# Kernel optimization log

Measured on AMD Instinct MI355X. Metric: run time of the kernel, lower is better.

## Reference

```python
import jax, jax.numpy as jnp
import numpy as np

LPOS, LDIR, H = 10, 4, 256
N = 262144


def posenc(x, L):
    freqs = (2.0 ** jnp.arange(L)).astype(x.dtype)  # [L]
    ang = x[:, None, :] * freqs[:, None]            # [N, L, 3]
    sc = jnp.concatenate([jnp.sin(ang), jnp.cos(ang)], axis=-1)  # [N, L, 6]
    return jnp.concatenate([x, sc.reshape(x.shape[0], L * 6)], axis=1)


def _lin(key, fan_in, fan_out):
    k1, k2 = jax.random.split(key)
    bound = 1.0 / np.sqrt(fan_in)
    w = jax.random.uniform(k1, (fan_out, fan_in), jnp.float32, -bound, bound)
    b = jax.random.uniform(k2, (fan_out,), jnp.float32, -bound, bound)
    return w, b


def setup_inputs() -> dict:
    key = jax.random.key(0)
    ks = jax.random.split(key, 16)
    inp = {
        'xyz': jax.random.normal(ks[0], (N, 3), jnp.float32),
        'd': jax.random.normal(ks[1], (N, 3), jnp.float32),
    }
    in1 = LPOS * 6 + 3  # 63
    dims1 = [(in1, H), (H, H), (H, H), (H, H), (H, H)]
    for i, (fi, fo) in enumerate(dims1):
        w, b = _lin(ks[2 + i], fi, fo)
        inp[f'w1_{i}'], inp[f'b1_{i}'] = w, b
    dims2 = [(H + in1, H), (H, H), (H, H), (H, H + 1)]
    for i, (fi, fo) in enumerate(dims2):
        w, b = _lin(ks[7 + i], fi, fo)
        inp[f'w2_{i}'], inp[f'b2_{i}'] = w, b
    w, b = _lin(ks[11], H + LDIR * 6 + 3, H // 2)
    inp['wr0'], inp['br0'] = w, b
    w, b = _lin(ks[12], H // 2, 3)
    inp['wr1'], inp['br1'] = w, b
    return inp


def reference(xyz, d,
              w1_0, b1_0, w1_1, b1_1, w1_2, b1_2, w1_3, b1_3, w1_4, b1_4,
              w2_0, b2_0, w2_1, b2_1, w2_2, b2_2, w2_3, b2_3,
              wr0, br0, wr1, br1):
    relu = jax.nn.relu
    x_emb = posenc(xyz, LPOS)  # [N, 63]
    d_emb = posenc(d, LDIR)    # [N, 27]
    h = x_emb
    for w, b in ((w1_0, b1_0), (w1_1, b1_1), (w1_2, b1_2), (w1_3, b1_3), (w1_4, b1_4)):
        h = relu(h @ w.T + b)
    h = jnp.concatenate([h, x_emb], axis=1)
    for w, b in ((w2_0, b2_0), (w2_1, b2_1), (w2_2, b2_2)):
        h = relu(h @ w.T + b)
    h = h @ w2_3.T + b2_3  # [N, H+1]
    sigma = h[:, -1]
    h = h[:, :-1]
    # rgb head
    g = relu(jnp.concatenate([h, d_emb], axis=1) @ wr0.T + br0)
    c = jax.nn.sigmoid(g @ wr1.T + br1)  # [N, 3]
    return c, relu(sigma)
```

## Files before the change

kernel.cpp:

```cpp
#include <hip/hip_runtime.h>
#include <hip/hip_bf16.h>

#define NPTS 262144
#define ROWS 64
#define BUF1_OFF 16384
#define XBUF_OFF 32768
#define LDS_BYTES ((16384*2 + 4096)*2)

typedef __attribute__((ext_vector_type(8)))  short short8;
typedef __attribute__((ext_vector_type(4)))  float f32x4;
typedef __attribute__((ext_vector_type(16))) float f32x16;

__device__ __forceinline__ ushort bfu(float f) {
  union { float f; unsigned u; } x; x.f = f;
  unsigned r = x.u + 0x7fffu + ((x.u >> 16) & 1u);
  return (ushort)(r >> 16);
}
__device__ __forceinline__ unsigned pk2(float a, float b) {
  __hip_bfloat162 h = __float22bfloat162_rn(float2{a, b});
  return *reinterpret_cast<unsigned*>(&h);
}

__global__ void pack_w(const float* __restrict__ w, ushort* __restrict__ dst,
                       int OUT, int KIN, int nct, int nkt) {
  int t = blockIdx.x * 256 + threadIdx.x;
  int total = nct * nkt * 64;
  if (t >= total) return;
  int l  = t & 63;
  int kt = (t >> 6) % nkt;
  int ct = (t >> 6) / nkt;
  int row = ct * 32 + (l & 31);
  int k0  = kt * 16 + (l >> 5) * 8;
  ushort* d = dst + (size_t)t * 8;
  #pragma unroll
  for (int j = 0; j < 8; ++j) {
    int k = k0 + j;
    float v = (row < OUT && k < KIN) ? w[(size_t)row * KIN + k] : 0.f;
    d[j] = bfu(v);
  }
}

__global__ void pack_b(const float* __restrict__ b, float* __restrict__ dst, int OUT, int OUTP) {
  int i = blockIdx.x * 256 + threadIdx.x;
  if (i < OUTP) dst[i] = (i < OUT) ? b[i] : 0.f;
}

template<int NKT, int KSPLIT, int NR, bool RELU>
__device__ __forceinline__ void layerg(
    const ushort* __restrict__ wpk, const float* __restrict__ bias,
    const ushort* a0, int s0, const ushort* a1, int s1,
    ushort* dst, int ct, int r2base, int lane)
{
  const int l5 = lane >> 5;
  f32x4 bq[4];
  #pragma unroll
  for (int qq = 0; qq < 4; ++qq)
    bq[qq] = *(const f32x4*)(bias + ct * 32 + qq * 8 + 4 * l5);
  f32x16 acc[NR];
  #pragma unroll
  for (int rr = 0; rr < NR; ++rr)
    #pragma unroll
    for (int qq = 0; qq < 4; ++qq) {
      acc[rr][qq * 4 + 0] = bq[qq][0];
      acc[rr][qq * 4 + 1] = bq[qq][1];
      acc[rr][qq * 4 + 2] = bq[qq][2];
      acc[rr][qq * 4 + 3] = bq[qq][3];
    }
  #pragma unroll
  for (int kt = 0; kt < NKT; ++kt) {
    short8 bv = *(const short8*)(wpk + (size_t)((ct * NKT + kt) * 64 + lane) * 8);
    #pragma unroll
    for (int rr = 0; rr < NR; ++rr) {
      const int r2 = r2base + rr;
      const ushort* src = (kt < KSPLIT)
          ? a0 + (r2 * s0 + kt) * 512 + lane * 8
          : a1 + (r2 * s1 + (kt - KSPLIT)) * 512 + lane * 8;
      short8 av = *(const short8*)src;
      acc[rr] = __builtin_amdgcn_mfma_f32_32x32x16_bf16(bv, av, acc[rr], 0, 0, 0);
    }
  }
  #pragma unroll
  for (int rr = 0; rr < NR; ++rr) {
    const int r2 = r2base + rr;
    #pragma unroll
    for (int qq = 0; qq < 4; ++qq) {
      float v0 = acc[rr][qq * 4 + 0], v1 = acc[rr][qq * 4 + 1];
      float v2 = acc[rr][qq * 4 + 2], v3 = acc[rr][qq * 4 + 3];
      if (RELU) {
        v0 = fmaxf(v0, 0.f); v1 = fmaxf(v1, 0.f);
        v2 = fmaxf(v2, 0.f); v3 = fmaxf(v3, 0.f);
      }
      uint2 p; p.x = pk2(v0, v1); p.y = pk2(v2, v3);
      *(uint2*)(dst + (r2 * 16 + ct * 2 + (qq >> 1)) * 512
                    + ((lane & 31) + 32 * (qq & 1)) * 8 + 4 * l5) = p;
    }
  }
}

__device__ __forceinline__ float pe_val(const float xv[3], int c, int CMAX) {
  if (c < 3) return xv[c];
  if (c < CMAX) {
    int idx = c - 3, l = idx / 6, t = idx - l * 6;
    float f = (float)(1 << l);
    float xx = xv[t < 3 ? t : t - 3];
    return (t < 3) ? __sinf(xx * f) : __cosf(xx * f);
  }
  return 0.f;
}

extern __shared__ ushort smem[];

__global__ __launch_bounds__(512, 4) void nerf_fused(
    const float* __restrict__ xyz, const float* __restrict__ dvec,
    const ushort* __restrict__ wp, const float* __restrict__ bp,
    float* __restrict__ out)
{
  ushort* buf0 = smem;
  ushort* buf1 = smem + BUF1_OFF;
  ushort* xbuf = smem + XBUF_OFF;
  const int tid  = threadIdx.x;
  const int row0 = blockIdx.x * ROWS;
  const int wave = tid >> 6, lane = tid & 63;
  const int l5 = lane >> 5;

  {
    const int r2 = wave >> 2, kt = wave & 3;
    const float* x = xyz + (size_t)(row0 + r2 * 32 + (lane & 31)) * 3;
    float xv[3] = {x[0], x[1], x[2]};
    const int c0 = kt * 16 + l5 * 8;
    unsigned u[4];
    #pragma unroll
    for (int q = 0; q < 4; ++q)
      u[q] = (unsigned)bfu(pe_val(xv, c0 + q * 2, 63))
           | ((unsigned)bfu(pe_val(xv, c0 + q * 2 + 1, 63)) << 16);
    *(uint4*)(xbuf + (r2 * 4 + kt) * 512 + lane * 8) = make_uint4(u[0], u[1], u[2], u[3]);
  }
  __syncthreads();
  layerg<4, 0, 2, true >(wp + 0,      bp + 0,    xbuf, 4, xbuf, 4, buf0, wave, 0, lane);
  __syncthreads();
  layerg<16, 16, 2, true>(wp + 16384,  bp + 256,  buf0, 16, buf0, 16, buf1, wave, 0, lane);
  __syncthreads();
  layerg<16, 16, 2, true>(wp + 81920,  bp + 512,  buf1, 16, buf1, 16, buf0, wave, 0, lane);
  __syncthreads();
  layerg<16, 16, 2, true>(wp + 147456, bp + 768,  buf0, 16, buf0, 16, buf1, wave, 0, lane);
  __syncthreads();
  layerg<16, 16, 2, true>(wp + 212992, bp + 1024, buf1, 16, buf1, 16, buf0, wave, 0, lane);
  __syncthreads();
  layerg<20, 16, 2, true>(wp + 278528, bp + 1280, buf0, 16, xbuf, 4, buf1, wave, 0, lane);
  __syncthreads();
  if (wave < 4) {
    const int r2 = wave >> 1, kt = wave & 1;
    const float* d = dvec + (size_t)(row0 + r2 * 32 + (lane & 31)) * 3;
    float dv[3] = {d[0], d[1], d[2]};
    const int c0 = kt * 16 + l5 * 8;
    unsigned u[4];
    #pragma unroll
    for (int q = 0; q < 4; ++q)
      u[q] = (unsigned)bfu(pe_val(dv, c0 + q * 2, 27))
           | ((unsigned)bfu(pe_val(dv, c0 + q * 2 + 1, 27)) << 16);
    *(uint4*)(xbuf + (r2 * 2 + kt) * 512 + lane * 8) = make_uint4(u[0], u[1], u[2], u[3]);
  }
  layerg<16, 16, 2, true>(wp + 360448, bp + 1536, buf1, 16, buf1, 16, buf0, wave, 0, lane);
  __syncthreads();
  layerg<16, 16, 2, true>(wp + 425984, bp + 1792, buf0, 16, buf0, 16, buf1, wave, 0, lane);
  __syncthreads();
  layerg<16, 16, 2, false>(wp + 491520, bp + 2048, buf1, 16, buf1, 16, buf0, wave, 0, lane);
  if (wave < 2) {
    const ushort* w23 = wp + 491520;
    const int r2 = wave;
    f32x16 acc;
    #pragma unroll
    for (int qq = 0; qq < 4; ++qq) {
      f32x4 b4 = *(const f32x4*)(bp + 2048 + 256 + qq * 8 + 4 * l5);
      acc[qq * 4 + 0] = b4[0]; acc[qq * 4 + 1] = b4[1];
      acc[qq * 4 + 2] = b4[2]; acc[qq * 4 + 3] = b4[3];
    }
    #pragma unroll
    for (int kt = 0; kt < 16; ++kt) {
      short8 bv = *(const short8*)(w23 + (size_t)((8 * 16 + kt) * 64 + lane) * 8);
      short8 av = *(const short8*)(buf1 + (r2 * 16 + kt) * 512 + lane * 8);
      acc = __builtin_amdgcn_mfma_f32_32x32x16_bf16(bv, av, acc, 0, 0, 0);
    }
    if (lane < 32)
      out[(size_t)3 * NPTS + row0 + r2 * 32 + lane] = fmaxf(acc[0], 0.f);
  }
  __syncthreads();
  layerg<18, 16, 1, true>(wp + 565248, bp + 2336, buf0, 16, xbuf, 2, buf1, wave & 3, wave >> 2, lane);
  __syncthreads();
  if (wave < 2) {
    const ushort* w = wp + 602112;
    const int r2 = wave;
    f32x16 acc;
    #pragma unroll
    for (int qq = 0; qq < 4; ++qq) {
      f32x4 b4 = *(const f32x4*)(bp + 2464 + qq * 8 + 4 * l5);
      acc[qq * 4 + 0] = b4[0]; acc[qq * 4 + 1] = b4[1];
      acc[qq * 4 + 2] = b4[2]; acc[qq * 4 + 3] = b4[3];
    }
    #pragma unroll
    for (int kt = 0; kt < 8; ++kt) {
      short8 bv = *(const short8*)(w + (size_t)(kt * 64 + lane) * 8);
      short8 av = *(const short8*)(buf1 + (r2 * 16 + kt) * 512 + lane * 8);
      acc = __builtin_amdgcn_mfma_f32_32x32x16_bf16(bv, av, acc, 0, 0, 0);
    }
    if (lane < 32) {
      int p = row0 + r2 * 32 + lane;
      out[(size_t)p * 3 + 0] = 1.f / (1.f + __expf(-acc[0]));
      out[(size_t)p * 3 + 1] = 1.f / (1.f + __expf(-acc[1]));
      out[(size_t)p * 3 + 2] = 1.f / (1.f + __expf(-acc[2]));
    }
  }
}

extern "C" void kernel_launch(void* const* d_in, const int* in_sizes, int n_in,
                              void* d_out, int out_size, void* d_ws, size_t ws_size,
                              hipStream_t stream) {
  const float* xyz  = (const float*)d_in[0];
  const float* dvec = (const float*)d_in[1];
  ushort* wp = (ushort*)d_ws;
  float*  bp = (float*)((char*)d_ws + 1212416);

  struct WSpec { int idx, OUT, KIN, nct, nkt, off; };
  const WSpec wspecs[11] = {
    { 2, 256,  63, 8,  4,      0},
    { 4, 256, 256, 8, 16,  16384},
    { 6, 256, 256, 8, 16,  81920},
    { 8, 256, 256, 8, 16, 147456},
    {10, 256, 256, 8, 16, 212992},
    {12, 256, 319, 8, 20, 278528},
    {14, 256, 256, 8, 16, 360448},
    {16, 256, 256, 8, 16, 425984},
    {18, 257, 256, 9, 16, 491520},
    {20, 128, 283, 4, 18, 565248},
    {22,   3, 128, 1,  8, 602112},
  };
  for (int i = 0; i < 11; ++i) {
    int total = wspecs[i].nct * wspecs[i].nkt * 64;
    pack_w<<<dim3((total + 255) / 256), dim3(256), 0, stream>>>(
      (const float*)d_in[wspecs[i].idx], wp + wspecs[i].off,
      wspecs[i].OUT, wspecs[i].KIN, wspecs[i].nct, wspecs[i].nkt);
  }
  struct BSpec { int idx, OUT, OUTP, off; };
  const BSpec bspecs[11] = {
    { 3, 256, 256,    0}, { 5, 256, 256,  256}, { 7, 256, 256,  512}, { 9, 256, 256,  768},
    {11, 256, 256, 1024}, {13, 256, 256, 1280}, {15, 256, 256, 1536}, {17, 256, 256, 1792},
    {19, 257, 288, 2048}, {21, 128, 128, 2336}, {23,   3,  32, 2464},
  };
  for (int i = 0; i < 11; ++i) {
    pack_b<<<dim3((bspecs[i].OUTP + 255) / 256), dim3(256), 0, stream>>>(
      (const float*)d_in[bspecs[i].idx], bp + bspecs[i].off, bspecs[i].OUT, bspecs[i].OUTP);
  }

  hipFuncSetAttribute(reinterpret_cast<const void*>(nerf_fused),
                      hipFuncAttributeMaxDynamicSharedMemorySize, LDS_BYTES);
  nerf_fused<<<dim3(NPTS / ROWS), dim3(512), LDS_BYTES, stream>>>(xyz, dvec, wp, bp, (float*)d_out);
}
```

Before: 380.3 us.

## Use 4 waves per block with two column tiles per wave for register reuse

Block size drops from 512 to 256 threads, and each wave now computes two 32-column output tiles for both 32-row groups. Each activation fragment loaded from LDS is reused across two weight tiles, which halves LDS activation reads per MFMA. The cost is twice the accumulator registers per wave (four 16-float accumulators) and fewer waves per block to hide latency. Launch bounds change to (256,2), which may lower occupancy.

```diff
diff --git a/kernel.cpp b/kernel.cpp
--- a/kernel.cpp
+++ b/kernel.cpp
@@ -45,54 +45,64 @@
   if (i < OUTP) dst[i] = (i < OUT) ? b[i] : 0.f;
 }
 
-template<int NKT, int KSPLIT, int NR, bool RELU>
+template<int NKT, int KSPLIT, int NCT, int NR, bool RELU>
 __device__ __forceinline__ void layerg(
     const ushort* __restrict__ wpk, const float* __restrict__ bias,
     const ushort* a0, int s0, const ushort* a1, int s1,
-    ushort* dst, int ct, int r2base, int lane)
+    ushort* dst, int ctBase, int r2base, int lane)
 {
   const int l5 = lane >> 5;
-  f32x4 bq[4];
-  #pragma unroll
-  for (int qq = 0; qq < 4; ++qq)
-    bq[qq] = *(const f32x4*)(bias + ct * 32 + qq * 8 + 4 * l5);
-  f32x16 acc[NR];
-  #pragma unroll
-  for (int rr = 0; rr < NR; ++rr)
+  f32x16 acc[NCT][NR];
+  #pragma unroll
+  for (int c = 0; c < NCT; ++c) {
     #pragma unroll
     for (int qq = 0; qq < 4; ++qq) {
-      acc[rr][qq * 4 + 0] = bq[qq][0];
-      acc[rr][qq * 4 + 1] = bq[qq][1];
-      acc[rr][qq * 4 + 2] = bq[qq][2];
-      acc[rr][qq * 4 + 3] = bq[qq][3];
-    }
+      f32x4 b4 = *(const f32x4*)(bias + (ctBase + c) * 32 + qq * 8 + 4 * l5);
+      #pragma unroll
+      for (int rr = 0; rr < NR; ++rr) {
+        acc[c][rr][qq * 4 + 0] = b4[0];
+        acc[c][rr][qq * 4 + 1] = b4[1];
+        acc[c][rr][qq * 4 + 2] = b4[2];
+        acc[c][rr][qq * 4 + 3] = b4[3];
+      }
+    }
+  }
   #pragma unroll
   for (int kt = 0; kt < NKT; ++kt) {
-    short8 bv = *(const short8*)(wpk + (size_t)((ct * NKT + kt) * 64 + lane) * 8);
+    short8 av[NR];
     #pragma unroll
     for (int rr = 0; rr < NR; ++rr) {
       const int r2 = r2base + rr;
-      const ushort* src = (kt < KSPLIT)
-          ? a0 + (r2 * s0 + kt) * 512 + lane * 8
-          : a1 + (r2 * s1 + (kt - KSPLIT)) * 512 + lane * 8;
-      short8 av = *(const short8*)src;
-      acc[rr] = __builtin_amdgcn_mfma_f32_32x32x16_bf16(bv, av, acc[rr], 0, 0, 0);
-    }
-  }
-  #pragma unroll
-  for (int rr = 0; rr < NR; ++rr) {
-    const int r2 = r2base + rr;
-    #pragma unroll
-    for (int qq = 0; qq < 4; ++qq) {
-      float v0 = acc[rr][qq * 4 + 0], v1 = acc[rr][qq * 4 + 1];
-      float v2 = acc[rr][qq * 4 + 2], v3 = acc[rr][qq * 4 + 3];
-      if (RELU) {
-        v0 = fmaxf(v0, 0.f); v1 = fmaxf(v1, 0.f);
-        v2 = fmaxf(v2, 0.f); v3 = fmaxf(v3, 0.f);
+      av[rr] = (kt < KSPLIT)
+        ? *(const short8*)(a0 + (size_t)(r2 * s0 + kt) * 512 + lane * 8)
+        : *(const short8*)(a1 + (size_t)(r2 * s1 + (kt - KSPLIT)) * 512 + lane * 8);
+    }
+    #pragma unroll
+    for (int c = 0; c < NCT; ++c) {
+      short8 bv = *(const short8*)(wpk + (size_t)(((ctBase + c) * NKT + kt) * 64 + lane) * 8);
+      #pragma unroll
+      for (int rr = 0; rr < NR; ++rr)
+        acc[c][rr] = __builtin_amdgcn_mfma_f32_32x32x16_bf16(bv, av[rr], acc[c][rr], 0, 0, 0);
+    }
+  }
+  #pragma unroll
+  for (int c = 0; c < NCT; ++c) {
+    const int ct = ctBase + c;
+    #pragma unroll
+    for (int rr = 0; rr < NR; ++rr) {
+      const int r2 = r2base + rr;
+      #pragma unroll
+      for (int qq = 0; qq < 4; ++qq) {
+        float v0 = acc[c][rr][qq * 4 + 0], v1 = acc[c][rr][qq * 4 + 1];
+        float v2 = acc[c][rr][qq * 4 + 2], v3 = acc[c][rr][qq * 4 + 3];
+        if (RELU) {
+          v0 = fmaxf(v0, 0.f); v1 = fmaxf(v1, 0.f);
+          v2 = fmaxf(v2, 0.f); v3 = fmaxf(v3, 0.f);
+        }
+        uint2 p; p.x = pk2(v0, v1); p.y = pk2(v2, v3);
+        *(uint2*)(dst + (size_t)(r2 * 16 + ct * 2 + (qq >> 1)) * 512
+                      + ((lane & 31) + 32 * (qq & 1)) * 8 + 4 * l5) = p;
       }
-      uint2 p; p.x = pk2(v0, v1); p.y = pk2(v2, v3);
-      *(uint2*)(dst + (r2 * 16 + ct * 2 + (qq >> 1)) * 512
-                    + ((lane & 31) + 32 * (qq & 1)) * 8 + 4 * l5) = p;
     }
   }
 }
@@ -110,7 +120,7 @@
 
 extern __shared__ ushort smem[];
 
-__global__ __launch_bounds__(512, 4) void nerf_fused(
+__global__ __launch_bounds__(256, 2) void nerf_fused(
     const float* __restrict__ xyz, const float* __restrict__ dvec,
     const ushort* __restrict__ wp, const float* __restrict__ bp,
     float* __restrict__ out)
@@ -124,31 +134,36 @@
   const int l5 = lane >> 5;
 
   {
-    const int r2 = wave >> 2, kt = wave & 3;
+    const int r2 = wave >> 1;
     const float* x = xyz + (size_t)(row0 + r2 * 32 + (lane & 31)) * 3;
     float xv[3] = {x[0], x[1], x[2]};
-    const int c0 = kt * 16 + l5 * 8;
-    unsigned u[4];
-    #pragma unroll
-    for (int q = 0; q < 4; ++q)
-      u[q] = (unsigned)bfu(pe_val(xv, c0 + q * 2, 63))
-           | ((unsigned)bfu(pe_val(xv, c0 + q * 2 + 1, 63)) << 16);
-    *(uint4*)(xbuf + (r2 * 4 + kt) * 512 + lane * 8) = make_uint4(u[0], u[1], u[2], u[3]);
-  }
-  __syncthreads();
-  layerg<4, 0, 2, true >(wp + 0,      bp + 0,    xbuf, 4, xbuf, 4, buf0, wave, 0, lane);
-  __syncthreads();
-  layerg<16, 16, 2, true>(wp + 16384,  bp + 256,  buf0, 16, buf0, 16, buf1, wave, 0, lane);
-  __syncthreads();
-  layerg<16, 16, 2, true>(wp + 81920,  bp + 512,  buf1, 16, buf1, 16, buf0, wave, 0, lane);
-  __syncthreads();
-  layerg<16, 16, 2, true>(wp + 147456, bp + 768,  buf0, 16, buf0, 16, buf1, wave, 0, lane);
-  __syncthreads();
-  layerg<16, 16, 2, true>(wp + 212992, bp + 1024, buf1, 16, buf1, 16, buf0, wave, 0, lane);
-  __syncthreads();
-  layerg<20, 16, 2, true>(wp + 278528, bp + 1280, buf0, 16, xbuf, 4, buf1, wave, 0, lane);
-  __syncthreads();
-  if (wave < 4) {
+    #pragma unroll
+    for (int t = 0; t < 2; ++t) {
+      const int L = wave * 2 + t;
+      const int kt = L & 3;
+      const int c0 = kt * 16 + l5 * 8;
+      unsigned u[4];
+      #pragma unroll
+      for (int q = 0; q < 4; ++q)
+        u[q] = (unsigned)bfu(pe_val(xv, c0 + q * 2, 63))
+             | ((unsigned)bfu(pe_val(xv, c0 + q * 2 + 1, 63)) << 16);
+      *(uint4*)(xbuf + (size_t)L * 512 + lane * 8) = make_uint4(u[0], u[1], u[2], u[3]);
+    }
+  }
+  __syncthreads();
+  layerg<4, 0, 2, 2, true >(wp + 0,      bp + 0,    xbuf, 4, xbuf, 4, buf0, wave * 2, 0, lane);
+  __syncthreads();
+  layerg<16, 16, 2, 2, true>(wp + 16384,  bp + 256,  buf0, 16, buf0, 16, buf1, wave * 2, 0, lane);
+  __syncthreads();
+  layerg<16, 16, 2, 2, true>(wp + 81920,  bp + 512,  buf1, 16, buf1, 16, buf0, wave * 2, 0, lane);
+  __syncthreads();
+  layerg<16, 16, 2, 2, true>(wp + 147456, bp + 768,  buf0, 16, buf0, 16, buf1, wave * 2, 0, lane);
+  __syncthreads();
+  layerg<16, 16, 2, 2, true>(wp + 212992, bp + 1024, buf1, 16, buf1, 16, buf0, wave * 2, 0, lane);
+  __syncthreads();
+  layerg<20, 16, 2, 2, true>(wp + 278528, bp + 1280, buf0, 16, xbuf, 4, buf1, wave * 2, 0, lane);
+  __syncthreads();
+  {
     const int r2 = wave >> 1, kt = wave & 1;
     const float* d = dvec + (size_t)(row0 + r2 * 32 + (lane & 31)) * 3;
     float dv[3] = {d[0], d[1], d[2]};
@@ -158,13 +173,13 @@
     for (int q = 0; q < 4; ++q)
       u[q] = (unsigned)bfu(pe_val(dv, c0 + q * 2, 27))
            | ((unsigned)bfu(pe_val(dv, c0 + q * 2 + 1, 27)) << 16);
-    *(uint4*)(xbuf + (r2 * 2 + kt) * 512 + lane * 8) = make_uint4(u[0], u[1], u[2], u[3]);
-  }
-  layerg<16, 16, 2, true>(wp + 360448, bp + 1536, buf1, 16, buf1, 16, buf0, wave, 0, lane);
-  __syncthreads();
-  layerg<16, 16, 2, true>(wp + 425984, bp + 1792, buf0, 16, buf0, 16, buf1, wave, 0, lane);
-  __syncthreads();
-  layerg<16, 16, 2, false>(wp + 491520, bp + 2048, buf1, 16, buf1, 16, buf0, wave, 0, lane);
+    *(uint4*)(xbuf + (size_t)(r2 * 2 + kt) * 512 + lane * 8) = make_uint4(u[0], u[1], u[2], u[3]);
+  }
+  layerg<16, 16, 2, 2, true>(wp + 360448, bp + 1536, buf1, 16, buf1, 16, buf0, wave * 2, 0, lane);
+  __syncthreads();
+  layerg<16, 16, 2, 2, true>(wp + 425984, bp + 1792, buf0, 16, buf0, 16, buf1, wave * 2, 0, lane);
+  __syncthreads();
+  layerg<16, 16, 2, 2, false>(wp + 491520, bp + 2048, buf1, 16, buf1, 16, buf0, wave * 2, 0, lane);
   if (wave < 2) {
     const ushort* w23 = wp + 491520;
     const int r2 = wave;
@@ -178,14 +193,14 @@
     #pragma unroll
     for (int kt = 0; kt < 16; ++kt) {
       short8 bv = *(const short8*)(w23 + (size_t)((8 * 16 + kt) * 64 + lane) * 8);
-      short8 av = *(const short8*)(buf1 + (r2 * 16 + kt) * 512 + lane * 8);
+      short8 av = *(const short8*)(buf1 + (size_t)(r2 * 16 + kt) * 512 + lane * 8);
       acc = __builtin_amdgcn_mfma_f32_32x32x16_bf16(bv, av, acc, 0, 0, 0);
     }
     if (lane < 32)
       out[(size_t)3 * NPTS + row0 + r2 * 32 + lane] = fmaxf(acc[0], 0.f);
   }
   __syncthreads();
-  layerg<18, 16, 1, true>(wp + 565248, bp + 2336, buf0, 16, xbuf, 2, buf1, wave & 3, wave >> 2, lane);
+  layerg<18, 16, 1, 2, true>(wp + 565248, bp + 2336, buf0, 16, xbuf, 2, buf1, wave, 0, lane);
   __syncthreads();
   if (wave < 2) {
     const ushort* w = wp + 602112;
@@ -200,7 +215,7 @@
     #pragma unroll
     for (int kt = 0; kt < 8; ++kt) {
       short8 bv = *(const short8*)(w + (size_t)(kt * 64 + lane) * 8);
-      short8 av = *(const short8*)(buf1 + (r2 * 16 + kt) * 512 + lane * 8);
+      short8 av = *(const short8*)(buf1 + (size_t)(r2 * 16 + kt) * 512 + lane * 8);
       acc = __builtin_amdgcn_mfma_f32_32x32x16_bf16(bv, av, acc, 0, 0, 0);
     }
     if (lane < 32) {
@@ -253,5 +268,5 @@
 
   hipFuncSetAttribute(reinterpret_cast<const void*>(nerf_fused),
                       hipFuncAttributeMaxDynamicSharedMemorySize, LDS_BYTES);
-  nerf_fused<<<dim3(NPTS / ROWS), dim3(512), LDS_BYTES, stream>>>(xyz, dvec, wp, bp, (float*)d_out);
-}
+  nerf_fused<<<dim3(NPTS / ROWS), dim3(256), LDS_BYTES, stream>>>(xyz, dvec, wp, bp, (float*)d_out);
+}
```

Result: slower. 455.3 us (+19.7%).
